# Kernel tuning notes

Hardware: AMD Instinct MI355X
Metric: run time of the kernel (lower is better)

## Reference

```python
import jax, jax.numpy as jnp
import numpy as np

K = 3
PAD = 1
STRIDE = 1
DIL = 1


def _bilinear_gather(feat, y, x):
    # feat: [B,C,H,W]; y,x: [B,KK,H,W] sampling coords -> [B,C,KK,H,W]
    B, C, H, W = feat.shape
    feat_flat = feat.reshape(B, C, H * W)
    y0 = jnp.floor(y)
    x0 = jnp.floor(x)
    out = jnp.zeros((B, C) + y.shape[1:], feat.dtype)
    for yi in (y0, y0 + 1.0):
        for xi in (x0, x0 + 1.0):
            wgt = (1.0 - jnp.abs(y - yi)) * (1.0 - jnp.abs(x - xi))
            valid = (yi >= 0) & (yi <= H - 1) & (xi >= 0) & (xi <= W - 1)
            yc = jnp.clip(yi, 0, H - 1).astype(jnp.int32)
            xc = jnp.clip(xi, 0, W - 1).astype(jnp.int32)
            idx = (yc * W + xc).reshape(B, 1, -1)  # [B,1,KK*H*W]
            g = jnp.take_along_axis(feat_flat, idx, axis=2).reshape(B, C, *y.shape[1:])
            out = out + g * (wgt * valid)[:, None]
    return out


def setup_inputs() -> dict:
    key = jax.random.key(0)
    k1, k2, k3, k4, k5 = jax.random.split(key, 5)
    B, Cin, Cout, H, W = 2, 256, 256, 96, 96
    x = jax.random.normal(k1, (B, Cin, H, W), jnp.float32)
    pw_w = jax.random.normal(k2, (Cout, Cin), jnp.float32) / np.sqrt(Cin)
    off_w = jax.random.normal(k3, (2 * K * K, Cout), jnp.float32) * 0.01
    off_b = jax.random.normal(k4, (2 * K * K,), jnp.float32) * 0.5
    dw_w = jax.random.normal(k5, (Cout, K, K), jnp.float32) / K
    return {"x": x, "pw_w": pw_w, "off_w": off_w, "off_b": off_b, "dw_w": dw_w}


def reference(x, pw_w, off_w, off_b, dw_w):
    B, _, H, W = x.shape
    C = pw_w.shape[0]
    # pointwise 1x1 conv (in_channels -> out_channels)
    xp = jnp.einsum("bchw,oc->bohw", x, pw_w)
    # offset 1x1 conv: [B, 2*K*K, H, W], layout (y,x) interleaved per kernel pos
    off = jnp.einsum("bchw,oc->bohw", xp, off_w) + off_b[None, :, None, None]
    off = off.reshape(B, K * K, 2, H, W)
    oy, ox = off[:, :, 0], off[:, :, 1]  # [B,KK,H,W]
    # base sampling grid per kernel position (stride 1, pad 1, dil 1)
    ky, kx = jnp.meshgrid(jnp.arange(K), jnp.arange(K), indexing="ij")
    ky = ky.reshape(-1).astype(jnp.float32)  # [KK]
    kx = kx.reshape(-1).astype(jnp.float32)
    gh = jnp.arange(H, dtype=jnp.float32) * STRIDE - PAD
    gw = jnp.arange(W, dtype=jnp.float32) * STRIDE - PAD
    base_y = gh[None, :, None] + (ky * DIL)[:, None, None]  # [KK,H,1]
    base_x = gw[None, None, :] + (kx * DIL)[:, None, None].transpose(0, 2, 1)  # [KK,1,W]
    y = base_y[None] + oy  # [B,KK,H,W]
    xc = base_x[None] + ox
    sampled = _bilinear_gather(xp, y, xc)  # [B,C,KK,H,W]
    out = jnp.einsum("bckhw,ck->bchw", sampled, dw_w.reshape(C, K * K))
    return out
```

## Files before the change

### kernel.cpp

```cpp
#include <hip/hip_runtime.h>
#include <hip/hip_bf16.h>

#define HWP 9216
#define HH  96
#define WW  96
#define CC  256
#define NB  2

typedef __attribute__((ext_vector_type(8))) short bf16x8;
typedef __attribute__((ext_vector_type(4))) float f32x4;

__device__ inline unsigned short f2bf(float f) {
  union { __hip_bfloat16 h; unsigned short u; } cvt;
  cvt.h = __float2bfloat16(f);
  return cvt.u;
}
__device__ inline float bf_lo(unsigned int u) { return __uint_as_float(u << 16); }
__device__ inline float bf_hi(unsigned int u) { return __uint_as_float(u & 0xffff0000u); }


__global__ __launch_bounds__(256) void k_main(const float* __restrict__ x,
                                              const float* __restrict__ pw_w,
                                              const float* __restrict__ off_w,
                                              const float* __restrict__ off_b,
                                              unsigned short* __restrict__ xpb,
                                              float* __restrict__ offs) {
  __shared__ unsigned short As[2][32 * 40];
  __shared__ unsigned short Bs[2][256 * 40];

  int g   = blockIdx.x;
  int e   = g & 7;
  int idx = g >> 3;
  int b   = idx / 36;
  int m   = idx - b * 36;
  int pix0 = (e * 36 + m) * 32;

  int t    = threadIdx.x;
  int lane = t & 63;
  int w    = t >> 6;
  int mw = (w & 1) * 16;
  int nw = (w >> 1) * 128;
  int r = lane & 15, q = lane >> 4;

  f32x4 acc[8] = {};

  const float* xg = x + (size_t)b * CC * HWP + pix0;
  int sc = t >> 3;
  int sp = (t & 7) * 4;
  int nB = t >> 2;
  int c8 = (t & 3) * 8;

  {
    f32x4 xv = __builtin_nontemporal_load((const f32x4*)(xg + (size_t)sc * HWP + sp));
    As[0][(sp + 0) * 40 + sc] = f2bf(xv.x);
    As[0][(sp + 1) * 40 + sc] = f2bf(xv.y);
    As[0][(sp + 2) * 40 + sc] = f2bf(xv.z);
    As[0][(sp + 3) * 40 + sc] = f2bf(xv.w);
#pragma unroll
    for (int rep = 0; rep < 4; ++rep) {
      int n = rep * 64 + nB;
      const float* wp = pw_w + n * 256 + c8;
      float4 w0 = *(const float4*)wp;
      float4 w1 = *(const float4*)(wp + 4);
      union { ushort4 h[2]; uint4 q4; } pk;
      pk.h[0] = make_ushort4(f2bf(w0.x), f2bf(w0.y), f2bf(w0.z), f2bf(w0.w));
      pk.h[1] = make_ushort4(f2bf(w1.x), f2bf(w1.y), f2bf(w1.z), f2bf(w1.w));
      *(uint4*)&Bs[0][n * 40 + c8] = pk.q4;
    }
  }
  __syncthreads();

  for (int kt = 0; kt < 8; ++kt) {
    int cur = kt & 1;
    f32x4 xv;
    float4 b0[4], b1[4];
    bool pre = (kt < 7);
    if (pre) {
      int k0 = (kt + 1) * 32;
      xv = __builtin_nontemporal_load((const f32x4*)(xg + (size_t)(k0 + sc) * HWP + sp));
#pragma unroll
      for (int rep = 0; rep < 4; ++rep) {
        const float* wp = pw_w + (rep * 64 + nB) * 256 + k0 + c8;
        b0[rep] = *(const float4*)wp;
        b1[rep] = *(const float4*)(wp + 4);
      }
    }
    bf16x8 a = *(const bf16x8*)&As[cur][(mw + r) * 40 + q * 8];
#pragma unroll
    for (int nt = 0; nt < 8; ++nt) {
      bf16x8 bb = *(const bf16x8*)&Bs[cur][(nw + nt * 16 + r) * 40 + q * 8];
      acc[nt] = __builtin_amdgcn_mfma_f32_16x16x32_bf16(a, bb, acc[nt], 0, 0, 0);
    }
    if (pre) {
      int nx = cur ^ 1;
      As[nx][(sp + 0) * 40 + sc] = f2bf(xv.x);
      As[nx][(sp + 1) * 40 + sc] = f2bf(xv.y);
      As[nx][(sp + 2) * 40 + sc] = f2bf(xv.z);
      As[nx][(sp + 3) * 40 + sc] = f2bf(xv.w);
#pragma unroll
      for (int rep = 0; rep < 4; ++rep) {
        int n = rep * 64 + nB;
        union { ushort4 h[2]; uint4 q4; } pk;
        pk.h[0] = make_ushort4(f2bf(b0[rep].x), f2bf(b0[rep].y), f2bf(b0[rep].z), f2bf(b0[rep].w));
        pk.h[1] = make_ushort4(f2bf(b1[rep].x), f2bf(b1[rep].y), f2bf(b1[rep].z), f2bf(b1[rep].w));
        *(uint4*)&Bs[nx][n * 40 + c8] = pk.q4;
      }
    }
    __syncthreads();
  }

  unsigned short* Cs = &Bs[0][0];

#pragma unroll
  for (int nt = 0; nt < 8; ++nt)
#pragma unroll
    for (int rr = 0; rr < 4; ++rr)
      Cs[(mw + q * 4 + rr) * 264 + nw + nt * 16 + r] = f2bf(acc[nt][rr]);
  __syncthreads();

  {
    int pix = t >> 3, c32 = (t & 7) * 32;
    unsigned short* o = xpb + ((size_t)b * HWP + pix0 + pix) * CC + c32;
#pragma unroll
    for (int j = 0; j < 4; ++j)
      *(uint4*)(o + j * 8) = *(const uint4*)&Cs[pix * 264 + c32 + j * 8];
  }

  {
    int mw2 = (w & 1) * 16;
    int nw2 = (w >> 1) * 16;
    int row = nw2 + r;
    f32x4 oacc = {};
#pragma unroll
    for (int ks = 0; ks < CC; ks += 32) {
      bf16x8 a = *(const bf16x8*)&Cs[(mw2 + r) * 264 + ks + q * 8];
      bf16x8 bb = {};
      if (row < 18) {
        const float* wp = off_w + row * 256 + ks + q * 8;
        float4 w0 = *(const float4*)wp;
        float4 w1 = *(const float4*)(wp + 4);
        union { unsigned short u[8]; bf16x8 v; } pk;
        pk.u[0] = f2bf(w0.x); pk.u[1] = f2bf(w0.y); pk.u[2] = f2bf(w0.z); pk.u[3] = f2bf(w0.w);
        pk.u[4] = f2bf(w1.x); pk.u[5] = f2bf(w1.y); pk.u[6] = f2bf(w1.z); pk.u[7] = f2bf(w1.w);
        bb = pk.v;
      }
      oacc = __builtin_amdgcn_mfma_f32_16x16x32_bf16(a, bb, oacc, 0, 0, 0);
    }
    if (row < 18) {
      float ob = off_b[row];
      size_t base = ((size_t)b * HWP + pix0 + mw2 + q * 4) * 20 + row;
#pragma unroll
      for (int rr = 0; rr < 4; ++rr)
        offs[base + (size_t)rr * 20] = oacc[rr] + ob;
    }
  }
}

__global__ __launch_bounds__(256) void k_gather(const unsigned short* __restrict__ xp,
                                                const float* __restrict__ offs,
                                                const float* __restrict__ dw_w,
                                                float* __restrict__ out) {
  __shared__ float Cs[8][257];
  __shared__ float4 Wt[8][9];
  __shared__ int4   Ad[8][9];
  __shared__ float  dvs[9][257];

  int g   = blockIdx.x;
  int e   = g & 7;
  int idx = g >> 3;
  int b   = idx / 144;
  int m2  = idx - b * 144;
  int c   = e * 144 + m2;
  int hw0 = c * 8;
  int pix0 = b * HWP + hw0;

  int wave = threadIdx.x >> 6;
  int lane = threadIdx.x & 63;
  int hp   = lane >> 5;
  int hl   = lane & 31;
  int ip   = wave * 2 + hp;
  int c0   = hl * 8;

  const unsigned short* xb = xp + (size_t)b * HWP * CC;
  const float* opb = offs + (size_t)pix0 * 20;

  {
    int t = threadIdx.x;
#pragma unroll
    for (int kk = 0; kk < 9; ++kk)
      dvs[kk][t] = dw_w[t * 9 + kk];
  }

  {
    int tp = threadIdx.x;
    if (tp < 72) {
      int ipp = tp / 9;
      int kk = tp - ipp * 9;
      int hw = hw0 + ipp;
      int h = hw / WW;
      int wq = hw - h * WW;
      float2 o2 = *(const float2*)(opb + ipp * 20 + 2 * kk);
      float y = (float)(h + kk / 3 - 1) + o2.x;
      float x = (float)(wq + kk % 3 - 1) + o2.y;
      float y0f = floorf(y), x0f = floorf(x);
      float fy = y - y0f, fx = x - x0f;
      int y0 = (int)y0f, x0 = (int)x0f;
      int y1 = y0 + 1, x1 = x0 + 1;
      bool vy0 = (y0 >= 0) & (y0 < HH);
      bool vy1 = (y1 >= 0) & (y1 < HH);
      bool vx0 = (x0 >= 0) & (x0 < WW);
      bool vx1 = (x1 >= 0) & (x1 < WW);
      int y0c = y0 < 0 ? 0 : (y0 > HH - 1 ? HH - 1 : y0);
      int y1c = y1 < 0 ? 0 : (y1 > HH - 1 ? HH - 1 : y1);
      int x0c = x0 < 0 ? 0 : (x0 > WW - 1 ? WW - 1 : x0);
      int x1c = x1 < 0 ? 0 : (x1 > WW - 1 ? WW - 1 : x1);
      Wt[ipp][kk] = make_float4(
          (1.f - fy) * (1.f - fx) * ((vy0 && vx0) ? 1.f : 0.f),
          (1.f - fy) * fx         * ((vy0 && vx1) ? 1.f : 0.f),
          fy * (1.f - fx)         * ((vy1 && vx0) ? 1.f : 0.f),
          fy * fx                 * ((vy1 && vx1) ? 1.f : 0.f));
      Ad[ipp][kk] = make_int4((y0c * WW + x0c) * (CC * 2), (y0c * WW + x1c) * (CC * 2),
                              (y1c * WW + x0c) * (CC * 2), (y1c * WW + x1c) * (CC * 2));
    }
  }
  __syncthreads();

  const char* xbc = (const char*)xb;
  unsigned lb = (unsigned)(hl * 16);

  float acc[8] = {};
#pragma unroll
  for (int kk = 0; kk < 9; ++kk) {
    float4 dv0 = *(const float4*)&dvs[kk][c0];
    float4 dv1 = *(const float4*)&dvs[kk][c0 + 4];
    float4 wv = Wt[ip][kk];
    int4 av = Ad[ip][kk];
    uint4 u00 = *(const uint4*)(xbc + ((unsigned)av.x + lb));
    uint4 u01 = *(const uint4*)(xbc + ((unsigned)av.y + lb));
    uint4 u10 = *(const uint4*)(xbc + ((unsigned)av.z + lb));
    uint4 u11 = *(const uint4*)(xbc + ((unsigned)av.w + lb));
    const unsigned* p00 = (const unsigned*)&u00;
    const unsigned* p01 = (const unsigned*)&u01;
    const unsigned* p10 = (const unsigned*)&u10;
    const unsigned* p11 = (const unsigned*)&u11;
    float dvv[8] = {dv0.x, dv0.y, dv0.z, dv0.w, dv1.x, dv1.y, dv1.z, dv1.w};
#pragma unroll
    for (int j = 0; j < 4; ++j) {
      unsigned w00 = p00[j], w01 = p01[j], w10 = p10[j], w11 = p11[j];
      float slo = wv.x * bf_lo(w00) + wv.y * bf_lo(w01) + wv.z * bf_lo(w10) + wv.w * bf_lo(w11);
      float shi = wv.x * bf_hi(w00) + wv.y * bf_hi(w01) + wv.z * bf_hi(w10) + wv.w * bf_hi(w11);
      acc[2 * j]     += dvv[2 * j]     * slo;
      acc[2 * j + 1] += dvv[2 * j + 1] * shi;
    }
  }
  *(float4*)&Cs[ip][c0]     = make_float4(acc[0], acc[1], acc[2], acc[3]);
  *(float4*)&Cs[ip][c0 + 4] = make_float4(acc[4], acc[5], acc[6], acc[7]);
  __syncthreads();
  int ch = threadIdx.x;
  float* ob = out + (size_t)b * CC * HWP + (size_t)ch * HWP + hw0;
  *(float4*)(ob + 0) = make_float4(Cs[0][ch], Cs[1][ch], Cs[2][ch], Cs[3][ch]);
  *(float4*)(ob + 4) = make_float4(Cs[4][ch], Cs[5][ch], Cs[6][ch], Cs[7][ch]);
}

extern "C" void kernel_launch(void* const* d_in, const int* in_sizes, int n_in,
                              void* d_out, int out_size, void* d_ws, size_t ws_size,
                              hipStream_t stream) {
  (void)in_sizes; (void)n_in; (void)out_size; (void)ws_size;
  const float* x     = (const float*)d_in[0];
  const float* pw_w  = (const float*)d_in[1];
  const float* off_w = (const float*)d_in[2];
  const float* off_b = (const float*)d_in[3];
  const float* dw_w  = (const float*)d_in[4];
  float* out = (float*)d_out;

  char* ws = (char*)d_ws;
  unsigned short* xpb = (unsigned short*)ws;
  float* offs = (float*)(ws + 9437184);

  k_main  <<<576, 256, 0, stream>>>(x, pw_w, off_w, off_b, xpb, offs);
  k_gather<<<2304, 256, 0, stream>>>(xpb, offs, dw_w, out);
}
```

Measured before the change: 116.9 us.

## Split pointwise GEMM over N halves and compute offset conv inside gather kernel

```diff
diff --git a/kernel.cpp b/kernel.cpp
--- a/kernel.cpp
+++ b/kernel.cpp
@@ -21,51 +21,50 @@
 
 __global__ __launch_bounds__(256) void k_main(const float* __restrict__ x,
                                               const float* __restrict__ pw_w,
-                                              const float* __restrict__ off_w,
-                                              const float* __restrict__ off_b,
-                                              unsigned short* __restrict__ xpb,
-                                              float* __restrict__ offs) {
+                                              unsigned short* __restrict__ xpb) {
   __shared__ unsigned short As[2][32 * 40];
-  __shared__ unsigned short Bs[2][256 * 40];
-
-  int g   = blockIdx.x;
-  int e   = g & 7;
-  int idx = g >> 3;
-  int b   = idx / 36;
-  int m   = idx - b * 36;
+  __shared__ unsigned short Bs[2][128 * 40];
+
+  int g    = blockIdx.x;
+  int e    = g & 7;
+  int idx  = g >> 3;
+  int nh   = idx & 1;
+  int idx2 = idx >> 1;
+  int b    = idx2 / 36;
+  int m    = idx2 - b * 36;
   int pix0 = (e * 36 + m) * 32;
+  int nb0  = nh * 128;
 
   int t    = threadIdx.x;
   int lane = t & 63;
   int w    = t >> 6;
-  int mw = (w & 1) * 16;
-  int nw = (w >> 1) * 128;
+  int mw  = (w & 1) * 16;
+  int nwl = (w >> 1) * 64;
   int r = lane & 15, q = lane >> 4;
 
-  f32x4 acc[8] = {};
+  f32x4 acc[4] = {};
 
   const float* xg = x + (size_t)b * CC * HWP + pix0;
   int sc = t >> 3;
   int sp = (t & 7) * 4;
-  int nB = t >> 2;
-  int c8 = (t & 3) * 8;
-
-  {
-    f32x4 xv = __builtin_nontemporal_load((const f32x4*)(xg + (size_t)sc * HWP + sp));
+  int nB = t >> 1;
+  int kh = (t & 1) * 16;
+
+  {
+    f32x4 xv = *(const f32x4*)(xg + (size_t)sc * HWP + sp);
     As[0][(sp + 0) * 40 + sc] = f2bf(xv.x);
     As[0][(sp + 1) * 40 + sc] = f2bf(xv.y);
     As[0][(sp + 2) * 40 + sc] = f2bf(xv.z);
     As[0][(sp + 3) * 40 + sc] = f2bf(xv.w);
-#pragma unroll
-    for (int rep = 0; rep < 4; ++rep) {
-      int n = rep * 64 + nB;
-      const float* wp = pw_w + n * 256 + c8;
-      float4 w0 = *(const float4*)wp;
-      float4 w1 = *(const float4*)(wp + 4);
-      union { ushort4 h[2]; uint4 q4; } pk;
-      pk.h[0] = make_ushort4(f2bf(w0.x), f2bf(w0.y), f2bf(w0.z), f2bf(w0.w));
-      pk.h[1] = make_ushort4(f2bf(w1.x), f2bf(w1.y), f2bf(w1.z), f2bf(w1.w));
-      *(uint4*)&Bs[0][n * 40 + c8] = pk.q4;
+    const float* wp = pw_w + (size_t)(nb0 + nB) * 256 + kh;
+#pragma unroll
+    for (int h = 0; h < 2; ++h) {
+      float4 w0 = *(const float4*)(wp + h * 8);
+      float4 w1 = *(const float4*)(wp + h * 8 + 4);
+      union { ushort4 s[2]; uint4 q4; } pk;
+      pk.s[0] = make_ushort4(f2bf(w0.x), f2bf(w0.y), f2bf(w0.z), f2bf(w0.w));
+      pk.s[1] = make_ushort4(f2bf(w1.x), f2bf(w1.y), f2bf(w1.z), f2bf(w1.w));
+      *(uint4*)&Bs[0][nB * 40 + kh + h * 8] = pk.q4;
     }
   }
   __syncthreads();
@@ -73,22 +72,22 @@
   for (int kt = 0; kt < 8; ++kt) {
     int cur = kt & 1;
     f32x4 xv;
-    float4 b0[4], b1[4];
+    float4 b0[2], b1[2];
     bool pre = (kt < 7);
     if (pre) {
       int k0 = (kt + 1) * 32;
-      xv = __builtin_nontemporal_load((const f32x4*)(xg + (size_t)(k0 + sc) * HWP + sp));
-#pragma unroll
-      for (int rep = 0; rep < 4; ++rep) {
-        const float* wp = pw_w + (rep * 64 + nB) * 256 + k0 + c8;
-        b0[rep] = *(const float4*)wp;
-        b1[rep] = *(const float4*)(wp + 4);
+      xv = *(const f32x4*)(xg + (size_t)(k0 + sc) * HWP + sp);
+      const float* wp = pw_w + (size_t)(nb0 + nB) * 256 + k0 + kh;
+#pragma unroll
+      for (int h = 0; h < 2; ++h) {
+        b0[h] = *(const float4*)(wp + h * 8);
+        b1[h] = *(const float4*)(wp + h * 8 + 4);
       }
     }
     bf16x8 a = *(const bf16x8*)&As[cur][(mw + r) * 40 + q * 8];
 #pragma unroll
-    for (int nt = 0; nt < 8; ++nt) {
-      bf16x8 bb = *(const bf16x8*)&Bs[cur][(nw + nt * 16 + r) * 40 + q * 8];
+    for (int nt = 0; nt < 4; ++nt) {
+      bf16x8 bb = *(const bf16x8*)&Bs[cur][(nwl + nt * 16 + r) * 40 + q * 8];
       acc[nt] = __builtin_amdgcn_mfma_f32_16x16x32_bf16(a, bb, acc[nt], 0, 0, 0);
     }
     if (pre) {
@@ -98,12 +97,11 @@
       As[nx][(sp + 2) * 40 + sc] = f2bf(xv.z);
       As[nx][(sp + 3) * 40 + sc] = f2bf(xv.w);
 #pragma unroll
-      for (int rep = 0; rep < 4; ++rep) {
-        int n = rep * 64 + nB;
-        union { ushort4 h[2]; uint4 q4; } pk;
-        pk.h[0] = make_ushort4(f2bf(b0[rep].x), f2bf(b0[rep].y), f2bf(b0[rep].z), f2bf(b0[rep].w));
-        pk.h[1] = make_ushort4(f2bf(b1[rep].x), f2bf(b1[rep].y), f2bf(b1[rep].z), f2bf(b1[rep].w));
-        *(uint4*)&Bs[nx][n * 40 + c8] = pk.q4;
+      for (int h = 0; h < 2; ++h) {
+        union { ushort4 s[2]; uint4 q4; } pk;
+        pk.s[0] = make_ushort4(f2bf(b0[h].x), f2bf(b0[h].y), f2bf(b0[h].z), f2bf(b0[h].w));
+        pk.s[1] = make_ushort4(f2bf(b1[h].x), f2bf(b1[h].y), f2bf(b1[h].z), f2bf(b1[h].w));
+        *(uint4*)&Bs[nx][nB * 40 + kh + h * 8] = pk.q4;
       }
     }
     __syncthreads();
@@ -112,58 +110,30 @@
   unsigned short* Cs = &Bs[0][0];
 
 #pragma unroll
-  for (int nt = 0; nt < 8; ++nt)
+  for (int nt = 0; nt < 4; ++nt)
 #pragma unroll
     for (int rr = 0; rr < 4; ++rr)
-      Cs[(mw + q * 4 + rr) * 264 + nw + nt * 16 + r] = f2bf(acc[nt][rr]);
-  __syncthreads();
-
-  {
-    int pix = t >> 3, c32 = (t & 7) * 32;
-    unsigned short* o = xpb + ((size_t)b * HWP + pix0 + pix) * CC + c32;
-#pragma unroll
-    for (int j = 0; j < 4; ++j)
-      *(uint4*)(o + j * 8) = *(const uint4*)&Cs[pix * 264 + c32 + j * 8];
-  }
-
-  {
-    int mw2 = (w & 1) * 16;
-    int nw2 = (w >> 1) * 16;
-    int row = nw2 + r;
-    f32x4 oacc = {};
-#pragma unroll
-    for (int ks = 0; ks < CC; ks += 32) {
-      bf16x8 a = *(const bf16x8*)&Cs[(mw2 + r) * 264 + ks + q * 8];
-      bf16x8 bb = {};
-      if (row < 18) {
-        const float* wp = off_w + row * 256 + ks + q * 8;
-        float4 w0 = *(const float4*)wp;
-        float4 w1 = *(const float4*)(wp + 4);
-        union { unsigned short u[8]; bf16x8 v; } pk;
-        pk.u[0] = f2bf(w0.x); pk.u[1] = f2bf(w0.y); pk.u[2] = f2bf(w0.z); pk.u[3] = f2bf(w0.w);
-        pk.u[4] = f2bf(w1.x); pk.u[5] = f2bf(w1.y); pk.u[6] = f2bf(w1.z); pk.u[7] = f2bf(w1.w);
-        bb = pk.v;
-      }
-      oacc = __builtin_amdgcn_mfma_f32_16x16x32_bf16(a, bb, oacc, 0, 0, 0);
-    }
-    if (row < 18) {
-      float ob = off_b[row];
-      size_t base = ((size_t)b * HWP + pix0 + mw2 + q * 4) * 20 + row;
-#pragma unroll
-      for (int rr = 0; rr < 4; ++rr)
-        offs[base + (size_t)rr * 20] = oacc[rr] + ob;
-    }
+      Cs[(mw + q * 4 + rr) * 136 + nwl + nt * 16 + r] = f2bf(acc[nt][rr]);
+  __syncthreads();
+
+  {
+    int pix = t >> 3, c16 = (t & 7) * 16;
+    unsigned short* o = xpb + ((size_t)b * HWP + pix0 + pix) * CC + nb0 + c16;
+    *(uint4*)(o + 0) = *(const uint4*)&Cs[pix * 136 + c16 + 0];
+    *(uint4*)(o + 8) = *(const uint4*)&Cs[pix * 136 + c16 + 8];
   }
 }
 
 __global__ __launch_bounds__(256) void k_gather(const unsigned short* __restrict__ xp,
-                                                const float* __restrict__ offs,
+                                                const float* __restrict__ off_w,
+                                                const float* __restrict__ off_b,
                                                 const float* __restrict__ dw_w,
                                                 float* __restrict__ out) {
   __shared__ float Cs[8][257];
   __shared__ float4 Wt[8][9];
   __shared__ int4   Ad[8][9];
   __shared__ float  dvs[9][257];
+  __shared__ float  offv[8][20];
 
   int g   = blockIdx.x;
   int e   = g & 7;
@@ -173,6 +143,7 @@
   int c   = e * 144 + m2;
   int hw0 = c * 8;
   int pix0 = b * HWP + hw0;
+  (void)pix0;
 
   int wave = threadIdx.x >> 6;
   int lane = threadIdx.x & 63;
@@ -182,7 +153,6 @@
   int c0   = hl * 8;
 
   const unsigned short* xb = xp + (size_t)b * HWP * CC;
-  const float* opb = offs + (size_t)pix0 * 20;
 
   {
     int t = threadIdx.x;
@@ -190,6 +160,29 @@
     for (int kk = 0; kk < 9; ++kk)
       dvs[kk][t] = dw_w[t * 9 + kk];
   }
+
+  {
+    int tp = threadIdx.x;
+    if (tp < 144) {
+      int ipp = tp / 18;
+      int o   = tp - ipp * 18;
+      const unsigned short* xrow = xb + (size_t)(hw0 + ipp) * CC;
+      const float* wr = off_w + o * 256;
+      float a = 0.f;
+#pragma unroll 8
+      for (int ks = 0; ks < 32; ++ks) {
+        uint4 u = *(const uint4*)(xrow + ks * 8);
+        float4 w0 = *(const float4*)(wr + ks * 8);
+        float4 w1 = *(const float4*)(wr + ks * 8 + 4);
+        a += bf_lo(u.x) * w0.x + bf_hi(u.x) * w0.y +
+             bf_lo(u.y) * w0.z + bf_hi(u.y) * w0.w +
+             bf_lo(u.z) * w1.x + bf_hi(u.z) * w1.y +
+             bf_lo(u.w) * w1.z + bf_hi(u.w) * w1.w;
+      }
+      offv[ipp][o] = a + off_b[o];
+    }
+  }
+  __syncthreads();
 
   {
     int tp = threadIdx.x;
@@ -199,9 +192,8 @@
       int hw = hw0 + ipp;
       int h = hw / WW;
       int wq = hw - h * WW;
-      float2 o2 = *(const float2*)(opb + ipp * 20 + 2 * kk);
-      float y = (float)(h + kk / 3 - 1) + o2.x;
-      float x = (float)(wq + kk % 3 - 1) + o2.y;
+      float y = (float)(h + kk / 3 - 1) + offv[ipp][2 * kk];
+      float x = (float)(wq + kk % 3 - 1) + offv[ipp][2 * kk + 1];
       float y0f = floorf(y), x0f = floorf(x);
       float fy = y - y0f, fx = x - x0f;
       int y0 = (int)y0f, x0 = (int)x0f;
@@ -275,8 +267,7 @@
 
   char* ws = (char*)d_ws;
   unsigned short* xpb = (unsigned short*)ws;
-  float* offs = (float*)(ws + 9437184);
-
-  k_main  <<<576, 256, 0, stream>>>(x, pw_w, off_w, off_b, xpb, offs);
-  k_gather<<<2304, 256, 0, stream>>>(xpb, offs, dw_w, out);
-}
+
+  k_main  <<<1152, 256, 0, stream>>>(x, pw_w, xpb);
+  k_gather<<<2304, 256, 0, stream>>>(xpb, off_w, off_b, dw_w, out);
+}
```

Result: slower. 152.6 us (+30.5%).
